# Performance work log

Hardware: AMD Instinct MI355X
Metric: run time of the kernel (lower is better)

## Reference

```python
import jax, jax.numpy as jnp
import numpy as np


def setup_inputs() -> dict:
    key = jax.random.key(0)
    B, C, H, W = 8, 64, 64, 64
    x = jax.random.normal(key, (B, C, H, W), dtype=jnp.float32)
    return {"x": x}


def reference(x) -> jnp.ndarray:
    # x: (B, C, H, W). Spatial self-attention over N = H*W positions with
    # Q = K = V = flattened x, no scaling, no projections (the Conv2d in the
    # original __init__ is never used in forward).
    B, C, H, W = x.shape
    N = H * W
    f = x.reshape(B, C, N)  # (B, C, N)
    # att[b, n, m] = sum_c f[b, c, n] * f[b, c, m]  -> (B, N, N)
    att = jnp.einsum('bcn,bcm->bnm', f, f)
    att = jax.nn.softmax(att, axis=-1)
    # outp[b, c, n] = sum_m f[b, c, m] * att[b, n, m]^T  (f_x @ att)
    outp = jnp.einsum('bcm,bmn->bcn', f, att).reshape(B, C, H, W)
    return x + outp
```

## Files before the change

### kernel.cpp

```cpp
#include <hip/hip_runtime.h>

typedef short v8s __attribute__((ext_vector_type(8)));
typedef short v4s __attribute__((ext_vector_type(4)));
typedef float v4f __attribute__((ext_vector_type(4)));

#define LOG2E 1.44269504088896340736f

#define WS_FBF_T 0u
#define WS_FBF   4194304u
#define WS_G     8388608u
#define WS_BMAX  8519680u
#define WS_NEED  8521728u

__device__ __forceinline__ unsigned short f2bf_rne(float f) {
  unsigned int u = __builtin_bit_cast(unsigned int, f);
  u += 0x7FFFu + ((u >> 16) & 1u);
  return (unsigned short)(u >> 16);
}

__global__ __launch_bounds__(256) void prep_kernel(
    const float* __restrict__ x, unsigned short* __restrict__ fbf_t,
    unsigned short* __restrict__ fbf, float* __restrict__ g, float* __restrict__ bmax) {
  __shared__ unsigned short T[64 * 72];
  __shared__ float red[16][64];
  const int t = threadIdx.x;
  const int b = blockIdx.x & 7;
  const int n0 = (blockIdx.x >> 3) << 6;
  const int nn = (t & 15) << 2;
  float ps0 = 0.f, ps1 = 0.f, ps2 = 0.f, ps3 = 0.f;
#pragma unroll
  for (int j = 0; j < 4; ++j) {
    int c = (t >> 4) + j * 16;
    size_t gidx = ((size_t)(b * 64 + c) << 12) + (unsigned)(n0 + nn);
    float4 v = *(const float4*)(x + gidx);
    ushort4 w;
    w.x = f2bf_rne(v.x); w.y = f2bf_rne(v.y); w.z = f2bf_rne(v.z); w.w = f2bf_rne(v.w);
    *(ushort4*)(fbf + gidx) = w;
    T[(nn + 0) * 72 + c] = w.x;
    T[(nn + 1) * 72 + c] = w.y;
    T[(nn + 2) * 72 + c] = w.z;
    T[(nn + 3) * 72 + c] = w.w;
    ps0 += v.x * v.x; ps1 += v.y * v.y; ps2 += v.z * v.z; ps3 += v.w * v.w;
  }
  red[t >> 4][nn + 0] = ps0; red[t >> 4][nn + 1] = ps1;
  red[t >> 4][nn + 2] = ps2; red[t >> 4][nn + 3] = ps3;
  __syncthreads();
  if (t < 64) {
    float gs = 0.f;
#pragma unroll
    for (int i = 0; i < 16; ++i) gs += red[i][t];
    g[b * 4096 + n0 + t] = gs;
    float m = gs;
    m = fmaxf(m, __shfl_xor(m, 1, 64));
    m = fmaxf(m, __shfl_xor(m, 2, 64));
    m = fmaxf(m, __shfl_xor(m, 4, 64));
    m = fmaxf(m, __shfl_xor(m, 8, 64));
    m = fmaxf(m, __shfl_xor(m, 16, 64));
    m = fmaxf(m, __shfl_xor(m, 32, 64));
    if (t == 0) bmax[b * 64 + (blockIdx.x >> 3)] = m;
  }
#pragma unroll
  for (int i = 0; i < 2; ++i) {
    int idx = t + i * 256;
    int n = idx >> 3, cs = (idx & 7) << 3;
    *(v8s*)(fbf_t + (((size_t)b << 12) + (unsigned)(n0 + n)) * 64 + cs) =
        *(const v8s*)&T[n * 72 + cs];
  }
}

__global__ __launch_bounds__(512, 2) void chanattn_main(
    const float* __restrict__ x, const unsigned short* __restrict__ fbf_t,
    const unsigned short* __restrict__ fbf, const float* __restrict__ g,
    const float* __restrict__ bmax, float* __restrict__ out) {
  __shared__ __align__(16) unsigned char smem[73728];
  unsigned short* sKtB = (unsigned short*)smem;
  unsigned short* sVcB = (unsigned short*)(smem + 18432);
  float* lred = (float*)(smem + 71680);
  const int BUF = 17920;

  const int tid = threadIdx.x;
  const int wave = tid >> 6, lane = tid & 63, quad = lane >> 4, l15 = lane & 15;
  const int qg = wave >> 2, kg = wave & 3;
  const int b = blockIdx.x & 7, qt = blockIdx.x >> 3;

  const unsigned short* fT = fbf_t + ((size_t)b << 18);
  const unsigned short* fV = fbf + ((size_t)b << 18);

  const int sKey = tid >> 3, sC = (tid & 7) << 3;
  const int vC = tid >> 4, vK = (tid & 15) << 3;
  const int vSlot = (vK & ~31) + ((vK & 8) ? 16 : 0) + ((vK & 16) ? 4 : 0);

  float gm = bmax[b * 64 + lane];
  gm = fmaxf(gm, __shfl_xor(gm, 1, 64));
  gm = fmaxf(gm, __shfl_xor(gm, 2, 64));
  gm = fmaxf(gm, __shfl_xor(gm, 4, 64));
  gm = fmaxf(gm, __shfl_xor(gm, 8, 64));
  gm = fmaxf(gm, __shfl_xor(gm, 16, 64));
  gm = fmaxf(gm, __shfl_xor(gm, 32, 64));
  float gq[4];
#pragma unroll
  for (int jq = 0; jq < 4; ++jq)
    gq[jq] = g[b * 4096 + qt * 128 + qg * 64 + jq * 16 + l15];

#pragma unroll
  for (int i = 0; i < 2; ++i)
    *(v8s*)&sKtB[(sKey + i * 64) * 72 + sC] =
        *(const v8s*)&fT[(size_t)(qt * 128 + sKey + i * 64) * 64 + sC];
  v8s pfk[2], pfv[2];
#pragma unroll
  for (int i = 0; i < 2; ++i)
    pfk[i] = *(const v8s*)&fT[(size_t)(sKey + i * 64) * 64 + sC];
#pragma unroll
  for (int i = 0; i < 2; ++i)
    pfv[i] = *(const v8s*)&fV[(size_t)(vC + i * 32) * 4096 + vK];

  __syncthreads();
  v8s bQ[4][2];
#pragma unroll
  for (int jq = 0; jq < 4; ++jq)
#pragma unroll
    for (int cs = 0; cs < 2; ++cs)
      bQ[jq][cs] = *(const v8s*)&sKtB[(qg * 64 + jq * 16 + l15) * 72 + cs * 32 + quad * 8];
  float msc[4];
#pragma unroll
  for (int jq = 0; jq < 4; ++jq) msc[jq] = __builtin_sqrtf(gq[jq] * gm) * LOG2E;
  __syncthreads();

#pragma unroll
  for (int i = 0; i < 2; ++i)
    *(v8s*)&sKtB[(sKey + i * 64) * 72 + sC] = pfk[i];
#pragma unroll
  for (int i = 0; i < 2; ++i) {
    v4s lo, hi;
#pragma unroll
    for (int j = 0; j < 4; ++j) { lo[j] = pfv[i][j]; hi[j] = pfv[i][j + 4]; }
    *(v4s*)&sVcB[(vC + i * 32) * 136 + vSlot] = lo;
    *(v4s*)&sVcB[(vC + i * 32) * 136 + vSlot + 8] = hi;
  }
#pragma unroll
  for (int i = 0; i < 2; ++i)
    pfk[i] = *(const v8s*)&fT[(size_t)(128 + sKey + i * 64) * 64 + sC];
#pragma unroll
  for (int i = 0; i < 2; ++i)
    pfv[i] = *(const v8s*)&fV[(size_t)(vC + i * 32) * 4096 + 128 + vK];

  v4f oacc[4][4];
  float rsum[4];
#pragma unroll
  for (int ct = 0; ct < 4; ++ct)
#pragma unroll
    for (int jq = 0; jq < 4; ++jq) oacc[ct][jq] = (v4f){0.f, 0.f, 0.f, 0.f};
#pragma unroll
  for (int jq = 0; jq < 4; ++jq) rsum[jq] = 0.f;

  for (int kt = 0; kt < 32; ++kt) {
    __syncthreads();
    const int po = (kt & 1) * BUF;
    const int pn = ((kt & 1) ^ 1) * BUF;

    v8s aK[2][2];
#pragma unroll
    for (int t = 0; t < 2; ++t)
#pragma unroll
      for (int cs = 0; cs < 2; ++cs)
        aK[t][cs] =
            *(const v8s*)&sKtB[po + (kg * 32 + t * 16 + l15) * 72 + cs * 32 + quad * 8];
    v8s aV[4];
#pragma unroll
    for (int ct = 0; ct < 4; ++ct)
      aV[ct] = *(const v8s*)&sVcB[po + (ct * 16 + l15) * 136 + kg * 32 + quad * 8];

    {
      const int jq = 0;
      v4f s0 = (v4f){0.f, 0.f, 0.f, 0.f}, s1 = (v4f){0.f, 0.f, 0.f, 0.f};
#pragma unroll
      for (int cs = 0; cs < 2; ++cs) {
        s0 = __builtin_amdgcn_mfma_f32_16x16x32_bf16(aK[0][cs], bQ[jq][cs], s0, 0, 0, 0);
        s1 = __builtin_amdgcn_mfma_f32_16x16x32_bf16(aK[1][cs], bQ[jq][cs], s1, 0, 0, 0);
      }
      float p0[4], p1[4];
#pragma unroll
      for (int r = 0; r < 4; ++r) {
        p0[r] = __builtin_amdgcn_exp2f(__builtin_fmaf(s0[r], LOG2E, -msc[jq]));
        p1[r] = __builtin_amdgcn_exp2f(__builtin_fmaf(s1[r], LOG2E, -msc[jq]));
      }
      rsum[jq] += ((p0[0] + p0[1]) + (p0[2] + p0[3])) +
                  ((p1[0] + p1[1]) + (p1[2] + p1[3]));
      uint4 up;
      up.x = (__builtin_bit_cast(unsigned int, p0[1]) & 0xFFFF0000u) |
             (__builtin_bit_cast(unsigned int, p0[0]) >> 16);
      up.y = (__builtin_bit_cast(unsigned int, p0[3]) & 0xFFFF0000u) |
             (__builtin_bit_cast(unsigned int, p0[2]) >> 16);
      up.z = (__builtin_bit_cast(unsigned int, p1[1]) & 0xFFFF0000u) |
             (__builtin_bit_cast(unsigned int, p1[0]) >> 16);
      up.w = (__builtin_bit_cast(unsigned int, p1[3]) & 0xFFFF0000u) |
             (__builtin_bit_cast(unsigned int, p1[2]) >> 16);
      v8s bp = __builtin_bit_cast(v8s, up);
#pragma unroll
      for (int ct = 0; ct < 4; ++ct)
        oacc[ct][jq] =
            __builtin_amdgcn_mfma_f32_16x16x32_bf16(aV[ct], bp, oacc[ct][jq], 0, 0, 0);
    }

    if (kt < 31) {
#pragma unroll
      for (int i = 0; i < 2; ++i)
        *(v8s*)&sKtB[pn + (sKey + i * 64) * 72 + sC] = pfk[i];
#pragma unroll
      for (int i = 0; i < 2; ++i) {
        v4s lo, hi;
#pragma unroll
        for (int j = 0; j < 4; ++j) { lo[j] = pfv[i][j]; hi[j] = pfv[i][j + 4]; }
        *(v4s*)&sVcB[pn + (vC + i * 32) * 136 + vSlot] = lo;
        *(v4s*)&sVcB[pn + (vC + i * 32) * 136 + vSlot + 8] = hi;
      }
    }
    if (kt < 30) {
      const int k0 = (kt + 2) << 7;
#pragma unroll
      for (int i = 0; i < 2; ++i)
        pfk[i] = *(const v8s*)&fT[(size_t)(k0 + sKey + i * 64) * 64 + sC];
#pragma unroll
      for (int i = 0; i < 2; ++i)
        pfv[i] = *(const v8s*)&fV[(size_t)(vC + i * 32) * 4096 + k0 + vK];
    }

#pragma unroll
    for (int jq = 1; jq < 4; ++jq) {
      v4f s0 = (v4f){0.f, 0.f, 0.f, 0.f}, s1 = (v4f){0.f, 0.f, 0.f, 0.f};
#pragma unroll
      for (int cs = 0; cs < 2; ++cs) {
        s0 = __builtin_amdgcn_mfma_f32_16x16x32_bf16(aK[0][cs], bQ[jq][cs], s0, 0, 0, 0);
        s1 = __builtin_amdgcn_mfma_f32_16x16x32_bf16(aK[1][cs], bQ[jq][cs], s1, 0, 0, 0);
      }
      float p0[4], p1[4];
#pragma unroll
      for (int r = 0; r < 4; ++r) {
        p0[r] = __builtin_amdgcn_exp2f(__builtin_fmaf(s0[r], LOG2E, -msc[jq]));
        p1[r] = __builtin_amdgcn_exp2f(__builtin_fmaf(s1[r], LOG2E, -msc[jq]));
      }
      rsum[jq] += ((p0[0] + p0[1]) + (p0[2] + p0[3])) +
                  ((p1[0] + p1[1]) + (p1[2] + p1[3]));
      uint4 up;
      up.x = (__builtin_bit_cast(unsigned int, p0[1]) & 0xFFFF0000u) |
             (__builtin_bit_cast(unsigned int, p0[0]) >> 16);
      up.y = (__builtin_bit_cast(unsigned int, p0[3]) & 0xFFFF0000u) |
             (__builtin_bit_cast(unsigned int, p0[2]) >> 16);
      up.z = (__builtin_bit_cast(unsigned int, p1[1]) & 0xFFFF0000u) |
             (__builtin_bit_cast(unsigned int, p1[0]) >> 16);
      up.w = (__builtin_bit_cast(unsigned int, p1[3]) & 0xFFFF0000u) |
             (__builtin_bit_cast(unsigned int, p1[2]) >> 16);
      v8s bp = __builtin_bit_cast(v8s, up);
#pragma unroll
      for (int ct = 0; ct < 4; ++ct)
        oacc[ct][jq] =
            __builtin_amdgcn_mfma_f32_16x16x32_bf16(aV[ct], bp, oacc[ct][jq], 0, 0, 0);
    }
  }

#pragma unroll
  for (int jq = 0; jq < 4; ++jq) {
    float s = rsum[jq];
    s += __shfl_xor(s, 16, 64);
    s += __shfl_xor(s, 32, 64);
    rsum[jq] = s;
  }
  if (quad == 0) {
#pragma unroll
    for (int jq = 0; jq < 4; ++jq)
      lred[(qg * 64 + jq * 16 + l15) * 4 + kg] = rsum[jq];
  }
  __syncthreads();
  float inv[4];
#pragma unroll
  for (int jq = 0; jq < 4; ++jq) {
    const float4 lv = *(const float4*)&lred[(qg * 64 + jq * 16 + l15) * 4];
    inv[jq] = __builtin_amdgcn_rcpf((lv.x + lv.y) + (lv.z + lv.w));
  }

  float* Obuf = (float*)smem;
#pragma unroll
  for (int round = 0; round < 4; ++round) {
    if (kg == round) {
#pragma unroll
      for (int ct = 0; ct < 4; ++ct)
#pragma unroll
        for (int jq = 0; jq < 4; ++jq)
#pragma unroll
          for (int r = 0; r < 4; ++r) {
            float val = oacc[ct][jq][r] * inv[jq];
            float* p = &Obuf[(qg * 64 + ct * 16 + quad * 4 + r) * 68 + jq * 16 + l15];
            if (round == 0) *p = val; else *p += val;
          }
    }
    __syncthreads();
  }
#pragma unroll
  for (int j = 0; j < 4; ++j) {
    int idx = tid + j * 512;
    int qg2 = idx >> 10, c = (idx >> 4) & 63, q4 = idx & 15;
    const float4 o = *(const float4*)&Obuf[(qg2 * 64 + c) * 68 + q4 * 4];
    size_t gidx = ((size_t)(b * 64 + c) << 12) + (unsigned)(qt * 128 + qg2 * 64 + q4 * 4);
    const float4 xv = *(const float4*)(x + gidx);
    float4 rv;
    rv.x = xv.x + o.x; rv.y = xv.y + o.y; rv.z = xv.z + o.z; rv.w = xv.w + o.w;
    *(float4*)(out + gidx) = rv;
  }
}

__global__ __launch_bounds__(512) void
chanattn_fallback(const float* __restrict__ x, float* __restrict__ out) {
  __shared__ __align__(16) unsigned char smem[54272];
  unsigned short* sKt = (unsigned short*)smem;
  unsigned short* sVc = (unsigned short*)(smem + 18432);
  unsigned short* sP  = (unsigned short*)(smem + 35840);
  const int tid = threadIdx.x;
  const int wave = tid >> 6, lane = tid & 63, quad = lane >> 4, l15 = lane & 15;
  const int b = blockIdx.x & 7, qt = blockIdx.x >> 3;
  const float* fb = x + (size_t)b * (64 * 4096);
  const int skey = tid & 127, sc0 = (tid >> 7) << 4;
  {
    float vq[16];
#pragma unroll
    for (int j = 0; j < 16; ++j) vq[j] = fb[(sc0 + j) * 4096 + qt * 128 + skey];
    unsigned short us[16];
#pragma unroll
    for (int j = 0; j < 16; ++j) us[j] = f2bf_rne(vq[j]);
#pragma unroll
    for (int h = 0; h < 2; ++h) {
      v8s t;
#pragma unroll
      for (int j = 0; j < 8; ++j) t[j] = (short)us[h * 8 + j];
      *(v8s*)&sKt[skey * 72 + sc0 + h * 8] = t;
    }
  }
  float vk[16];
#pragma unroll
  for (int j = 0; j < 16; ++j) vk[j] = fb[(sc0 + j) * 4096 + skey];
  __syncthreads();
  v8s aq[2];
#pragma unroll
  for (int cs = 0; cs < 2; ++cs)
    aq[cs] = *(const v8s*)&sKt[(wave * 16 + l15) * 72 + cs * 32 + quad * 8];
  __syncthreads();
  v4f oacc[4];
#pragma unroll
  for (int ct = 0; ct < 4; ++ct) oacc[ct] = (v4f){0.f, 0.f, 0.f, 0.f};
  float m_run[4], l_run[4];
#pragma unroll
  for (int r = 0; r < 4; ++r) { m_run[r] = -3.0e38f; l_run[r] = 0.f; }
  unsigned short* sPw = sP + wave * (16 * 72);
  for (int kt = 0; kt < 32; ++kt) {
    {
      unsigned short us[16];
#pragma unroll
      for (int j = 0; j < 16; ++j) us[j] = f2bf_rne(vk[j]);
#pragma unroll
      for (int h = 0; h < 2; ++h) {
        v8s t;
#pragma unroll
        for (int j = 0; j < 8; ++j) t[j] = (short)us[h * 8 + j];
        *(v8s*)&sKt[skey * 72 + sc0 + h * 8] = t;
      }
#pragma unroll
      for (int j = 0; j < 16; ++j) sVc[(sc0 + j) * 136 + skey] = us[j];
    }
    __syncthreads();
    if (kt + 1 < 32) {
      const int m0 = (kt + 1) * 128;
#pragma unroll
      for (int j = 0; j < 16; ++j) vk[j] = fb[(sc0 + j) * 4096 + m0 + skey];
    }
    v4f sacc[8];
#pragma unroll
    for (int t = 0; t < 8; ++t) {
      v4f acc = (v4f){0.f, 0.f, 0.f, 0.f};
#pragma unroll
      for (int cs = 0; cs < 2; ++cs) {
        v8s bf = *(const v8s*)&sKt[(t * 16 + l15) * 72 + cs * 32 + quad * 8];
        acc = __builtin_amdgcn_mfma_f32_16x16x32_bf16(aq[cs], bf, acc, 0, 0, 0);
      }
      sacc[t] = acc;
    }
    float alpha[4], msc[4], rsum[4];
#pragma unroll
    for (int r = 0; r < 4; ++r) {
      float mv = sacc[0][r];
#pragma unroll
      for (int t = 1; t < 8; ++t) mv = fmaxf(mv, sacc[t][r]);
      mv = fmaxf(mv, __shfl_xor(mv, 8, 64));
      mv = fmaxf(mv, __shfl_xor(mv, 4, 64));
      mv = fmaxf(mv, __shfl_xor(mv, 2, 64));
      mv = fmaxf(mv, __shfl_xor(mv, 1, 64));
      float mnew = fmaxf(m_run[r], mv);
      alpha[r] = __builtin_amdgcn_exp2f((m_run[r] - mnew) * LOG2E);
      m_run[r] = mnew;
      msc[r] = mnew * LOG2E;
      l_run[r] *= alpha[r];
      rsum[r] = 0.f;
    }
#pragma unroll
    for (int ct = 0; ct < 4; ++ct)
#pragma unroll
      for (int r = 0; r < 4; ++r) oacc[ct][r] *= alpha[r];
#pragma unroll
    for (int half = 0; half < 2; ++half) {
#pragma unroll
      for (int t = half * 4; t < half * 4 + 4; ++t)
#pragma unroll
        for (int r = 0; r < 4; ++r) {
          float p = __builtin_amdgcn_exp2f(__builtin_fmaf(sacc[t][r], LOG2E, -msc[r]));
          rsum[r] += p;
          sPw[(quad * 4 + r) * 72 + (t - half * 4) * 16 + l15] = f2bf_rne(p);
        }
      asm volatile("s_waitcnt lgkmcnt(0)" ::: "memory");
#pragma unroll
      for (int ms = 0; ms < 2; ++ms) {
        v8s af = *(const v8s*)&sPw[l15 * 72 + ms * 32 + quad * 8];
#pragma unroll
        for (int ct = 0; ct < 4; ++ct) {
          v8s bf = *(const v8s*)&sVc[(ct * 16 + l15) * 136 + (half * 2 + ms) * 32 + quad * 8];
          oacc[ct] = __builtin_amdgcn_mfma_f32_16x16x32_bf16(af, bf, oacc[ct], 0, 0, 0);
        }
      }
      asm volatile("s_waitcnt lgkmcnt(0)" ::: "memory");
    }
#pragma unroll
    for (int r = 0; r < 4; ++r) {
      float s = rsum[r];
      s += __shfl_xor(s, 8, 64);
      s += __shfl_xor(s, 4, 64);
      s += __shfl_xor(s, 2, 64);
      s += __shfl_xor(s, 1, 64);
      l_run[r] += s;
    }
    __syncthreads();
  }
  float inv[4];
#pragma unroll
  for (int r = 0; r < 4; ++r) inv[r] = __builtin_amdgcn_rcpf(l_run[r]);
  float* sOt = (float*)smem;
#pragma unroll
  for (int ct = 0; ct < 4; ++ct)
#pragma unroll
    for (int r = 0; r < 4; ++r)
      sOt[(ct * 16 + l15) * 132 + wave * 16 + quad * 4 + r] = oacc[ct][r] * inv[r];
  __syncthreads();
#pragma unroll
  for (int j = 0; j < 4; ++j) {
    int idx = tid + j * 512;
    int nv = idx & 31, c = idx >> 5;
    float4 o = *(const float4*)&sOt[c * 132 + nv * 4];
    size_t gaddr = (size_t)b * (64 * 4096) + (size_t)c * 4096 + (size_t)(qt * 128 + nv * 4);
    float4 xv = *(const float4*)(x + gaddr);
    float4 res = make_float4(xv.x + o.x, xv.y + o.y, xv.z + o.z, xv.w + o.w);
    *(float4*)(out + gaddr) = res;
  }
}

extern "C" void kernel_launch(void* const* d_in, const int* in_sizes, int n_in,
                              void* d_out, int out_size, void* d_ws, size_t ws_size,
                              hipStream_t stream) {
  const float* xin = (const float*)d_in[0];
  float* out = (float*)d_out;
  if (ws_size >= (size_t)WS_NEED) {
    unsigned short* fbf_t = (unsigned short*)((char*)d_ws + WS_FBF_T);
    unsigned short* fbf = (unsigned short*)((char*)d_ws + WS_FBF);
    float* g = (float*)((char*)d_ws + WS_G);
    float* bmax = (float*)((char*)d_ws + WS_BMAX);
    prep_kernel<<<dim3(512), dim3(256), 0, stream>>>(xin, fbf_t, fbf, g, bmax);
    chanattn_main<<<dim3(256), dim3(512), 0, stream>>>(xin, fbf_t, fbf, g, bmax, out);
  } else {
    chanattn_fallback<<<dim3(256), dim3(512), 0, stream>>>(xin, out);
  }
}
```

Measured before the change: 105.0 us.

## Use 1024-thread attention blocks with smaller per-wave query tiles; rewrite prep transpose

The main attention kernel now runs 1024 threads (16 waves) per block. Each wave handles 32 query rows instead of 64, which halves accumulator registers and spreads the cooperative tile loads over more threads. The prep kernel is rewritten so each thread processes one spatial position across 32 channels. That lets it write the transposed bf16 rows directly without a shared-memory transpose, and it uses 256 blocks and a 32-entry max table. Softmax probability packing now goes through a byte-permute builtin. The trade-off is one block per CU with a large shared-memory footprint, so there is less inter-block overlap, and the prep kernel's bf16 stores are strided 2-byte writes.

```diff
diff --git a/kernel.cpp b/kernel.cpp
--- a/kernel.cpp
+++ b/kernel.cpp
@@ -18,57 +18,66 @@
   return (unsigned short)(u >> 16);
 }
 
+__device__ __forceinline__ unsigned int pack_hi16(float hi, float lo) {
+#if defined(__has_builtin) && __has_builtin(__builtin_amdgcn_perm)
+  return __builtin_amdgcn_perm(__builtin_bit_cast(unsigned int, hi),
+                               __builtin_bit_cast(unsigned int, lo), 0x07060302u);
+#else
+  return (__builtin_bit_cast(unsigned int, hi) & 0xFFFF0000u) |
+         (__builtin_bit_cast(unsigned int, lo) >> 16);
+#endif
+}
+
 __global__ __launch_bounds__(256) void prep_kernel(
     const float* __restrict__ x, unsigned short* __restrict__ fbf_t,
     unsigned short* __restrict__ fbf, float* __restrict__ g, float* __restrict__ bmax) {
-  __shared__ unsigned short T[64 * 72];
-  __shared__ float red[16][64];
+  __shared__ float red[128];
+  __shared__ float wmax[2];
   const int t = threadIdx.x;
-  const int b = blockIdx.x & 7;
-  const int n0 = (blockIdx.x >> 3) << 6;
-  const int nn = (t & 15) << 2;
-  float ps0 = 0.f, ps1 = 0.f, ps2 = 0.f, ps3 = 0.f;
-#pragma unroll
-  for (int j = 0; j < 4; ++j) {
-    int c = (t >> 4) + j * 16;
-    size_t gidx = ((size_t)(b * 64 + c) << 12) + (unsigned)(n0 + nn);
-    float4 v = *(const float4*)(x + gidx);
-    ushort4 w;
-    w.x = f2bf_rne(v.x); w.y = f2bf_rne(v.y); w.z = f2bf_rne(v.z); w.w = f2bf_rne(v.w);
-    *(ushort4*)(fbf + gidx) = w;
-    T[(nn + 0) * 72 + c] = w.x;
-    T[(nn + 1) * 72 + c] = w.y;
-    T[(nn + 2) * 72 + c] = w.z;
-    T[(nn + 3) * 72 + c] = w.w;
-    ps0 += v.x * v.x; ps1 += v.y * v.y; ps2 += v.z * v.z; ps3 += v.w * v.w;
-  }
-  red[t >> 4][nn + 0] = ps0; red[t >> 4][nn + 1] = ps1;
-  red[t >> 4][nn + 2] = ps2; red[t >> 4][nn + 3] = ps3;
-  __syncthreads();
-  if (t < 64) {
-    float gs = 0.f;
-#pragma unroll
-    for (int i = 0; i < 16; ++i) gs += red[i][t];
-    g[b * 4096 + n0 + t] = gs;
-    float m = gs;
+  const int b = blockIdx.x & 7, nch = blockIdx.x >> 3;
+  const int n = (nch << 7) + (t & 127);
+  const int chalf = t >> 7, c0 = chalf << 5;
+
+  const float* xb = x + (((size_t)(b * 64 + c0)) << 12) + n;
+  unsigned short* fb = fbf + (((size_t)(b * 64 + c0)) << 12) + n;
+  float sq = 0.f;
+  unsigned int pk[16];
+#pragma unroll
+  for (int cc = 0; cc < 16; ++cc) {
+    float v0 = xb[(size_t)(2 * cc) << 12];
+    float v1 = xb[(size_t)(2 * cc + 1) << 12];
+    sq = __builtin_fmaf(v0, v0, sq);
+    sq = __builtin_fmaf(v1, v1, sq);
+    unsigned short w0 = f2bf_rne(v0), w1 = f2bf_rne(v1);
+    pk[cc] = (unsigned int)w0 | ((unsigned int)w1 << 16);
+    fb[(size_t)(2 * cc) << 12] = w0;
+    fb[(size_t)(2 * cc + 1) << 12] = w1;
+  }
+  unsigned short* ft = fbf_t + ((size_t)b << 18) + (size_t)n * 64 + c0;
+#pragma unroll
+  for (int k = 0; k < 4; ++k) {
+    uint4 u = make_uint4(pk[4 * k], pk[4 * k + 1], pk[4 * k + 2], pk[4 * k + 3]);
+    *(uint4*)(ft + k * 8) = u;
+  }
+  if (chalf == 0) red[t] = sq;
+  __syncthreads();
+  if (chalf == 1) {
+    float tot = sq + red[t & 127];
+    g[b * 4096 + n] = tot;
+    float m = tot;
     m = fmaxf(m, __shfl_xor(m, 1, 64));
     m = fmaxf(m, __shfl_xor(m, 2, 64));
     m = fmaxf(m, __shfl_xor(m, 4, 64));
     m = fmaxf(m, __shfl_xor(m, 8, 64));
     m = fmaxf(m, __shfl_xor(m, 16, 64));
     m = fmaxf(m, __shfl_xor(m, 32, 64));
-    if (t == 0) bmax[b * 64 + (blockIdx.x >> 3)] = m;
-  }
-#pragma unroll
-  for (int i = 0; i < 2; ++i) {
-    int idx = t + i * 256;
-    int n = idx >> 3, cs = (idx & 7) << 3;
-    *(v8s*)(fbf_t + (((size_t)b << 12) + (unsigned)(n0 + n)) * 64 + cs) =
-        *(const v8s*)&T[n * 72 + cs];
-  }
-}
-
-__global__ __launch_bounds__(512, 2) void chanattn_main(
+    if ((t & 63) == 0) wmax[(t >> 6) & 1] = m;
+  }
+  __syncthreads();
+  if (t == 0) bmax[b * 32 + nch] = fmaxf(wmax[0], wmax[1]);
+}
+
+__global__ __launch_bounds__(1024) void chanattn_main(
     const float* __restrict__ x, const unsigned short* __restrict__ fbf_t,
     const unsigned short* __restrict__ fbf, const float* __restrict__ g,
     const float* __restrict__ bmax, float* __restrict__ out) {
@@ -90,68 +99,52 @@
   const int vC = tid >> 4, vK = (tid & 15) << 3;
   const int vSlot = (vK & ~31) + ((vK & 8) ? 16 : 0) + ((vK & 16) ? 4 : 0);
 
-  float gm = bmax[b * 64 + lane];
+  float gm = bmax[b * 32 + (lane & 31)];
   gm = fmaxf(gm, __shfl_xor(gm, 1, 64));
   gm = fmaxf(gm, __shfl_xor(gm, 2, 64));
   gm = fmaxf(gm, __shfl_xor(gm, 4, 64));
   gm = fmaxf(gm, __shfl_xor(gm, 8, 64));
   gm = fmaxf(gm, __shfl_xor(gm, 16, 64));
-  gm = fmaxf(gm, __shfl_xor(gm, 32, 64));
-  float gq[4];
-#pragma unroll
-  for (int jq = 0; jq < 4; ++jq)
-    gq[jq] = g[b * 4096 + qt * 128 + qg * 64 + jq * 16 + l15];
-
-#pragma unroll
-  for (int i = 0; i < 2; ++i)
-    *(v8s*)&sKtB[(sKey + i * 64) * 72 + sC] =
-        *(const v8s*)&fT[(size_t)(qt * 128 + sKey + i * 64) * 64 + sC];
-  v8s pfk[2], pfv[2];
-#pragma unroll
-  for (int i = 0; i < 2; ++i)
-    pfk[i] = *(const v8s*)&fT[(size_t)(sKey + i * 64) * 64 + sC];
-#pragma unroll
-  for (int i = 0; i < 2; ++i)
-    pfv[i] = *(const v8s*)&fV[(size_t)(vC + i * 32) * 4096 + vK];
-
-  __syncthreads();
-  v8s bQ[4][2];
-#pragma unroll
-  for (int jq = 0; jq < 4; ++jq)
+  float gq[2];
+#pragma unroll
+  for (int jq = 0; jq < 2; ++jq)
+    gq[jq] = g[b * 4096 + qt * 128 + qg * 32 + jq * 16 + l15];
+
+  *(v8s*)&sKtB[sKey * 72 + sC] =
+      *(const v8s*)&fT[(size_t)(qt * 128 + sKey) * 64 + sC];
+  v8s pfk = *(const v8s*)&fT[(size_t)sKey * 64 + sC];
+  v8s pfv = *(const v8s*)&fV[(size_t)vC * 4096 + vK];
+
+  __syncthreads();
+  v8s bQ[2][2];
+#pragma unroll
+  for (int jq = 0; jq < 2; ++jq)
 #pragma unroll
     for (int cs = 0; cs < 2; ++cs)
-      bQ[jq][cs] = *(const v8s*)&sKtB[(qg * 64 + jq * 16 + l15) * 72 + cs * 32 + quad * 8];
-  float msc[4];
-#pragma unroll
-  for (int jq = 0; jq < 4; ++jq) msc[jq] = __builtin_sqrtf(gq[jq] * gm) * LOG2E;
-  __syncthreads();
-
-#pragma unroll
-  for (int i = 0; i < 2; ++i)
-    *(v8s*)&sKtB[(sKey + i * 64) * 72 + sC] = pfk[i];
-#pragma unroll
-  for (int i = 0; i < 2; ++i) {
+      bQ[jq][cs] = *(const v8s*)&sKtB[(qg * 32 + jq * 16 + l15) * 72 + cs * 32 + quad * 8];
+  float msc[2];
+#pragma unroll
+  for (int jq = 0; jq < 2; ++jq) msc[jq] = __builtin_sqrtf(gq[jq] * gm) * LOG2E;
+  __syncthreads();
+
+  *(v8s*)&sKtB[sKey * 72 + sC] = pfk;
+  {
     v4s lo, hi;
 #pragma unroll
-    for (int j = 0; j < 4; ++j) { lo[j] = pfv[i][j]; hi[j] = pfv[i][j + 4]; }
-    *(v4s*)&sVcB[(vC + i * 32) * 136 + vSlot] = lo;
-    *(v4s*)&sVcB[(vC + i * 32) * 136 + vSlot + 8] = hi;
-  }
-#pragma unroll
-  for (int i = 0; i < 2; ++i)
-    pfk[i] = *(const v8s*)&fT[(size_t)(128 + sKey + i * 64) * 64 + sC];
-#pragma unroll
-  for (int i = 0; i < 2; ++i)
-    pfv[i] = *(const v8s*)&fV[(size_t)(vC + i * 32) * 4096 + 128 + vK];
-
-  v4f oacc[4][4];
-  float rsum[4];
+    for (int j = 0; j < 4; ++j) { lo[j] = pfv[j]; hi[j] = pfv[j + 4]; }
+    *(v4s*)&sVcB[vC * 136 + vSlot] = lo;
+    *(v4s*)&sVcB[vC * 136 + vSlot + 8] = hi;
+  }
+  pfk = *(const v8s*)&fT[(size_t)(128 + sKey) * 64 + sC];
+  pfv = *(const v8s*)&fV[(size_t)vC * 4096 + 128 + vK];
+
+  v4f oacc[4][2];
+  float rsum[2];
 #pragma unroll
   for (int ct = 0; ct < 4; ++ct)
 #pragma unroll
-    for (int jq = 0; jq < 4; ++jq) oacc[ct][jq] = (v4f){0.f, 0.f, 0.f, 0.f};
-#pragma unroll
-  for (int jq = 0; jq < 4; ++jq) rsum[jq] = 0.f;
+    for (int jq = 0; jq < 2; ++jq) oacc[ct][jq] = (v4f){0.f, 0.f, 0.f, 0.f};
+  rsum[0] = 0.f; rsum[1] = 0.f;
 
   for (int kt = 0; kt < 32; ++kt) {
     __syncthreads();
@@ -187,14 +180,10 @@
       rsum[jq] += ((p0[0] + p0[1]) + (p0[2] + p0[3])) +
                   ((p1[0] + p1[1]) + (p1[2] + p1[3]));
       uint4 up;
-      up.x = (__builtin_bit_cast(unsigned int, p0[1]) & 0xFFFF0000u) |
-             (__builtin_bit_cast(unsigned int, p0[0]) >> 16);
-      up.y = (__builtin_bit_cast(unsigned int, p0[3]) & 0xFFFF0000u) |
-             (__builtin_bit_cast(unsigned int, p0[2]) >> 16);
-      up.z = (__builtin_bit_cast(unsigned int, p1[1]) & 0xFFFF0000u) |
-             (__builtin_bit_cast(unsigned int, p1[0]) >> 16);
-      up.w = (__builtin_bit_cast(unsigned int, p1[3]) & 0xFFFF0000u) |
-             (__builtin_bit_cast(unsigned int, p1[2]) >> 16);
+      up.x = pack_hi16(p0[1], p0[0]);
+      up.y = pack_hi16(p0[3], p0[2]);
+      up.z = pack_hi16(p1[1], p1[0]);
+      up.w = pack_hi16(p1[3], p1[2]);
       v8s bp = __builtin_bit_cast(v8s, up);
 #pragma unroll
       for (int ct = 0; ct < 4; ++ct)
@@ -203,30 +192,21 @@
     }
 
     if (kt < 31) {
-#pragma unroll
-      for (int i = 0; i < 2; ++i)
-        *(v8s*)&sKtB[pn + (sKey + i * 64) * 72 + sC] = pfk[i];
-#pragma unroll
-      for (int i = 0; i < 2; ++i) {
-        v4s lo, hi;
-#pragma unroll
-        for (int j = 0; j < 4; ++j) { lo[j] = pfv[i][j]; hi[j] = pfv[i][j + 4]; }
-        *(v4s*)&sVcB[pn + (vC + i * 32) * 136 + vSlot] = lo;
-        *(v4s*)&sVcB[pn + (vC + i * 32) * 136 + vSlot + 8] = hi;
-      }
+      *(v8s*)&sKtB[pn + sKey * 72 + sC] = pfk;
+      v4s lo, hi;
+#pragma unroll
+      for (int j = 0; j < 4; ++j) { lo[j] = pfv[j]; hi[j] = pfv[j + 4]; }
+      *(v4s*)&sVcB[pn + vC * 136 + vSlot] = lo;
+      *(v4s*)&sVcB[pn + vC * 136 + vSlot + 8] = hi;
     }
     if (kt < 30) {
       const int k0 = (kt + 2) << 7;
-#pragma unroll
-      for (int i = 0; i < 2; ++i)
-        pfk[i] = *(const v8s*)&fT[(size_t)(k0 + sKey + i * 64) * 64 + sC];
-#pragma unroll
-      for (int i = 0; i < 2; ++i)
-        pfv[i] = *(const v8s*)&fV[(size_t)(vC + i * 32) * 4096 + k0 + vK];
-    }
-
-#pragma unroll
-    for (int jq = 1; jq < 4; ++jq) {
+      pfk = *(const v8s*)&fT[(size_t)(k0 + sKey) * 64 + sC];
+      pfv = *(const v8s*)&fV[(size_t)vC * 4096 + k0 + vK];
+    }
+
+    {
+      const int jq = 1;
       v4f s0 = (v4f){0.f, 0.f, 0.f, 0.f}, s1 = (v4f){0.f, 0.f, 0.f, 0.f};
 #pragma unroll
       for (int cs = 0; cs < 2; ++cs) {
@@ -242,14 +222,10 @@
       rsum[jq] += ((p0[0] + p0[1]) + (p0[2] + p0[3])) +
                   ((p1[0] + p1[1]) + (p1[2] + p1[3]));
       uint4 up;
-      up.x = (__builtin_bit_cast(unsigned int, p0[1]) & 0xFFFF0000u) |
-             (__builtin_bit_cast(unsigned int, p0[0]) >> 16);
-      up.y = (__builtin_bit_cast(unsigned int, p0[3]) & 0xFFFF0000u) |
-             (__builtin_bit_cast(unsigned int, p0[2]) >> 16);
-      up.z = (__builtin_bit_cast(unsigned int, p1[1]) & 0xFFFF0000u) |
-             (__builtin_bit_cast(unsigned int, p1[0]) >> 16);
-      up.w = (__builtin_bit_cast(unsigned int, p1[3]) & 0xFFFF0000u) |
-             (__builtin_bit_cast(unsigned int, p1[2]) >> 16);
+      up.x = pack_hi16(p0[1], p0[0]);
+      up.y = pack_hi16(p0[3], p0[2]);
+      up.z = pack_hi16(p1[1], p1[0]);
+      up.w = pack_hi16(p1[3], p1[2]);
       v8s bp = __builtin_bit_cast(v8s, up);
 #pragma unroll
       for (int ct = 0; ct < 4; ++ct)
@@ -259,7 +235,7 @@
   }
 
 #pragma unroll
-  for (int jq = 0; jq < 4; ++jq) {
+  for (int jq = 0; jq < 2; ++jq) {
     float s = rsum[jq];
     s += __shfl_xor(s, 16, 64);
     s += __shfl_xor(s, 32, 64);
@@ -267,14 +243,14 @@
   }
   if (quad == 0) {
 #pragma unroll
-    for (int jq = 0; jq < 4; ++jq)
-      lred[(qg * 64 + jq * 16 + l15) * 4 + kg] = rsum[jq];
-  }
-  __syncthreads();
-  float inv[4];
-#pragma unroll
-  for (int jq = 0; jq < 4; ++jq) {
-    const float4 lv = *(const float4*)&lred[(qg * 64 + jq * 16 + l15) * 4];
+    for (int jq = 0; jq < 2; ++jq)
+      lred[(qg * 32 + jq * 16 + l15) * 4 + kg] = rsum[jq];
+  }
+  __syncthreads();
+  float inv[2];
+#pragma unroll
+  for (int jq = 0; jq < 2; ++jq) {
+    const float4 lv = *(const float4*)&lred[(qg * 32 + jq * 16 + l15) * 4];
     inv[jq] = __builtin_amdgcn_rcpf((lv.x + lv.y) + (lv.z + lv.w));
   }
 
@@ -285,22 +261,22 @@
 #pragma unroll
       for (int ct = 0; ct < 4; ++ct)
 #pragma unroll
-        for (int jq = 0; jq < 4; ++jq)
+        for (int jq = 0; jq < 2; ++jq)
 #pragma unroll
           for (int r = 0; r < 4; ++r) {
             float val = oacc[ct][jq][r] * inv[jq];
-            float* p = &Obuf[(qg * 64 + ct * 16 + quad * 4 + r) * 68 + jq * 16 + l15];
+            float* p = &Obuf[(ct * 16 + quad * 4 + r) * 132 + qg * 32 + jq * 16 + l15];
             if (round == 0) *p = val; else *p += val;
           }
     }
     __syncthreads();
   }
 #pragma unroll
-  for (int j = 0; j < 4; ++j) {
-    int idx = tid + j * 512;
-    int qg2 = idx >> 10, c = (idx >> 4) & 63, q4 = idx & 15;
-    const float4 o = *(const float4*)&Obuf[(qg2 * 64 + c) * 68 + q4 * 4];
-    size_t gidx = ((size_t)(b * 64 + c) << 12) + (unsigned)(qt * 128 + qg2 * 64 + q4 * 4);
+  for (int j = 0; j < 2; ++j) {
+    int idx = tid + j * 1024;
+    int c = idx >> 5, q4 = idx & 31;
+    const float4 o = *(const float4*)&Obuf[c * 132 + q4 * 4];
+    size_t gidx = ((size_t)(b * 64 + c) << 12) + (unsigned)(qt * 128 + q4 * 4);
     const float4 xv = *(const float4*)(x + gidx);
     float4 rv;
     rv.x = xv.x + o.x; rv.y = xv.y + o.y; rv.z = xv.z + o.z; rv.w = xv.w + o.w;
@@ -468,8 +444,8 @@
     unsigned short* fbf = (unsigned short*)((char*)d_ws + WS_FBF);
     float* g = (float*)((char*)d_ws + WS_G);
     float* bmax = (float*)((char*)d_ws + WS_BMAX);
-    prep_kernel<<<dim3(512), dim3(256), 0, stream>>>(xin, fbf_t, fbf, g, bmax);
-    chanattn_main<<<dim3(256), dim3(512), 0, stream>>>(xin, fbf_t, fbf, g, bmax, out);
+    prep_kernel<<<dim3(256), dim3(256), 0, stream>>>(xin, fbf_t, fbf, g, bmax);
+    chanattn_main<<<dim3(256), dim3(1024), 0, stream>>>(xin, fbf_t, fbf, g, bmax, out);
   } else {
     chanattn_fallback<<<dim3(256), dim3(512), 0, stream>>>(xin, out);
   }
```

New measurement: 106.5 us. Within noise of the previous version (+1.5%).

## Assign attention tiles per XCC via atomic claim and prepermute V layout in prep

Applied to the files above, without the earlier changes.

Each main-kernel block now claims a tile with an atomic CAS, starting from a range chosen by its XCC id, so that all 32 query tiles of one batch run on the same XCC and share its L2 for K/V reads. The prep kernel is rewritten to write V already in the slot-permuted layout the MFMA needs, which lets the main loop store V to LDS with a single 16-byte write instead of a split shuffle. Packing bf16 pairs now uses a v_perm builtin. The change adds a hipMemsetAsync launch and atomics, and the prep kernel now does strided 2-byte scattered global stores.

```diff
diff --git a/kernel.cpp b/kernel.cpp
--- a/kernel.cpp
+++ b/kernel.cpp
@@ -1,16 +1,16 @@
 #include <hip/hip_runtime.h>
 
 typedef short v8s __attribute__((ext_vector_type(8)));
-typedef short v4s __attribute__((ext_vector_type(4)));
 typedef float v4f __attribute__((ext_vector_type(4)));
 
 #define LOG2E 1.44269504088896340736f
 
 #define WS_FBF_T 0u
-#define WS_FBF   4194304u
+#define WS_FVP   4194304u
 #define WS_G     8388608u
 #define WS_BMAX  8519680u
-#define WS_NEED  8521728u
+#define WS_TAKEN 8521728u
+#define WS_NEED  8522752u
 
 __device__ __forceinline__ unsigned short f2bf_rne(float f) {
   unsigned int u = __builtin_bit_cast(unsigned int, f);
@@ -18,77 +18,96 @@
   return (unsigned short)(u >> 16);
 }
 
+__device__ __forceinline__ unsigned int pack_hi16(float hi, float lo) {
+#if defined(__has_builtin) && __has_builtin(__builtin_amdgcn_perm)
+  return __builtin_amdgcn_perm(__builtin_bit_cast(unsigned int, hi),
+                               __builtin_bit_cast(unsigned int, lo), 0x07060302u);
+#else
+  return (__builtin_bit_cast(unsigned int, hi) & 0xFFFF0000u) |
+         (__builtin_bit_cast(unsigned int, lo) >> 16);
+#endif
+}
+
+__device__ __forceinline__ int get_xcc_id() {
+  return (int)(__builtin_amdgcn_s_getreg((3 << 11) | 20) & 7u);
+}
+
 __global__ __launch_bounds__(256) void prep_kernel(
     const float* __restrict__ x, unsigned short* __restrict__ fbf_t,
-    unsigned short* __restrict__ fbf, float* __restrict__ g, float* __restrict__ bmax) {
-  __shared__ unsigned short T[64 * 72];
-  __shared__ float red[16][64];
+    unsigned short* __restrict__ fvp, float* __restrict__ g, float* __restrict__ bmax) {
+  __shared__ float red[4][64];
   const int t = threadIdx.x;
-  const int b = blockIdx.x & 7;
-  const int n0 = (blockIdx.x >> 3) << 6;
-  const int nn = (t & 15) << 2;
-  float ps0 = 0.f, ps1 = 0.f, ps2 = 0.f, ps3 = 0.f;
-#pragma unroll
-  for (int j = 0; j < 4; ++j) {
-    int c = (t >> 4) + j * 16;
-    size_t gidx = ((size_t)(b * 64 + c) << 12) + (unsigned)(n0 + nn);
-    float4 v = *(const float4*)(x + gidx);
-    ushort4 w;
-    w.x = f2bf_rne(v.x); w.y = f2bf_rne(v.y); w.z = f2bf_rne(v.z); w.w = f2bf_rne(v.w);
-    *(ushort4*)(fbf + gidx) = w;
-    T[(nn + 0) * 72 + c] = w.x;
-    T[(nn + 1) * 72 + c] = w.y;
-    T[(nn + 2) * 72 + c] = w.z;
-    T[(nn + 3) * 72 + c] = w.w;
-    ps0 += v.x * v.x; ps1 += v.y * v.y; ps2 += v.z * v.z; ps3 += v.w * v.w;
-  }
-  red[t >> 4][nn + 0] = ps0; red[t >> 4][nn + 1] = ps1;
-  red[t >> 4][nn + 2] = ps2; red[t >> 4][nn + 3] = ps3;
+  const int b = blockIdx.x & 7, ch = blockIdx.x >> 3;
+  const int n0 = ch << 6, nn = t & 63, n = n0 + nn, cg = t >> 6;
+
+  const int kin = nn & 31;
+  const int slot = (kin < 16) ? (((kin >> 2) << 3) + (kin & 3))
+                              : ((((kin - 16) >> 2) << 3) + ((kin - 16) & 3) + 4);
+  const int ncol = (n & ~31) + slot;
+
+  float sq = 0.f;
+  unsigned short w[16];
+#pragma unroll
+  for (int j = 0; j < 16; ++j) {
+    const int c = cg * 16 + j;
+    float v = x[((size_t)(b * 64 + c) << 12) + n];
+    sq = __builtin_fmaf(v, v, sq);
+    w[j] = f2bf_rne(v);
+  }
+  unsigned short* ft = fbf_t + ((size_t)b << 18) + (size_t)n * 64 + cg * 16;
+  *(v8s*)ft = *(v8s*)&w[0];
+  *(v8s*)(ft + 8) = *(v8s*)&w[8];
+#pragma unroll
+  for (int j = 0; j < 16; ++j)
+    fvp[((size_t)(b * 64 + cg * 16 + j) << 12) + ncol] = w[j];
+
+  red[cg][nn] = sq;
   __syncthreads();
   if (t < 64) {
-    float gs = 0.f;
-#pragma unroll
-    for (int i = 0; i < 16; ++i) gs += red[i][t];
-    g[b * 4096 + n0 + t] = gs;
-    float m = gs;
+    float tot = (red[0][t] + red[1][t]) + (red[2][t] + red[3][t]);
+    g[b * 4096 + n0 + t] = tot;
+    float m = tot;
     m = fmaxf(m, __shfl_xor(m, 1, 64));
     m = fmaxf(m, __shfl_xor(m, 2, 64));
     m = fmaxf(m, __shfl_xor(m, 4, 64));
     m = fmaxf(m, __shfl_xor(m, 8, 64));
     m = fmaxf(m, __shfl_xor(m, 16, 64));
     m = fmaxf(m, __shfl_xor(m, 32, 64));
-    if (t == 0) bmax[b * 64 + (blockIdx.x >> 3)] = m;
-  }
-#pragma unroll
-  for (int i = 0; i < 2; ++i) {
-    int idx = t + i * 256;
-    int n = idx >> 3, cs = (idx & 7) << 3;
-    *(v8s*)(fbf_t + (((size_t)b << 12) + (unsigned)(n0 + n)) * 64 + cs) =
-        *(const v8s*)&T[n * 72 + cs];
+    if (t == 0) bmax[b * 64 + ch] = m;
   }
 }
 
 __global__ __launch_bounds__(512, 2) void chanattn_main(
     const float* __restrict__ x, const unsigned short* __restrict__ fbf_t,
-    const unsigned short* __restrict__ fbf, const float* __restrict__ g,
-    const float* __restrict__ bmax, float* __restrict__ out) {
+    const unsigned short* __restrict__ fvp, const float* __restrict__ g,
+    const float* __restrict__ bmax, int* __restrict__ taken,
+    float* __restrict__ out) {
   __shared__ __align__(16) unsigned char smem[73728];
   unsigned short* sKtB = (unsigned short*)smem;
   unsigned short* sVcB = (unsigned short*)(smem + 18432);
   float* lred = (float*)(smem + 71680);
   const int BUF = 17920;
+  __shared__ int s_tile;
 
   const int tid = threadIdx.x;
   const int wave = tid >> 6, lane = tid & 63, quad = lane >> 4, l15 = lane & 15;
   const int qg = wave >> 2, kg = wave & 3;
-  const int b = blockIdx.x & 7, qt = blockIdx.x >> 3;
+
+  if (tid == 0) {
+    int start = (get_xcc_id() << 5);
+    int t = start;
+    while (atomicCAS(&taken[t], 0, 1) != 0) t = (t + 1) & 255;
+    s_tile = t;
+  }
+  __syncthreads();
+  const int tile = s_tile;
+  const int b = tile >> 5, qt = tile & 31;
 
   const unsigned short* fT = fbf_t + ((size_t)b << 18);
-  const unsigned short* fV = fbf + ((size_t)b << 18);
+  const unsigned short* fV = fvp + ((size_t)b << 18);
 
   const int sKey = tid >> 3, sC = (tid & 7) << 3;
   const int vC = tid >> 4, vK = (tid & 15) << 3;
-  const int vSlot = (vK & ~31) + ((vK & 8) ? 16 : 0) + ((vK & 16) ? 4 : 0);
 
   float gm = bmax[b * 64 + lane];
   gm = fmaxf(gm, __shfl_xor(gm, 1, 64));
@@ -130,13 +149,8 @@
   for (int i = 0; i < 2; ++i)
     *(v8s*)&sKtB[(sKey + i * 64) * 72 + sC] = pfk[i];
 #pragma unroll
-  for (int i = 0; i < 2; ++i) {
-    v4s lo, hi;
-#pragma unroll
-    for (int j = 0; j < 4; ++j) { lo[j] = pfv[i][j]; hi[j] = pfv[i][j + 4]; }
-    *(v4s*)&sVcB[(vC + i * 32) * 136 + vSlot] = lo;
-    *(v4s*)&sVcB[(vC + i * 32) * 136 + vSlot + 8] = hi;
-  }
+  for (int i = 0; i < 2; ++i)
+    *(v8s*)&sVcB[(vC + i * 32) * 136 + vK] = pfv[i];
 #pragma unroll
   for (int i = 0; i < 2; ++i)
     pfk[i] = *(const v8s*)&fT[(size_t)(128 + sKey + i * 64) * 64 + sC];
@@ -187,14 +201,10 @@
       rsum[jq] += ((p0[0] + p0[1]) + (p0[2] + p0[3])) +
                   ((p1[0] + p1[1]) + (p1[2] + p1[3]));
       uint4 up;
-      up.x = (__builtin_bit_cast(unsigned int, p0[1]) & 0xFFFF0000u) |
-             (__builtin_bit_cast(unsigned int, p0[0]) >> 16);
-      up.y = (__builtin_bit_cast(unsigned int, p0[3]) & 0xFFFF0000u) |
-             (__builtin_bit_cast(unsigned int, p0[2]) >> 16);
-      up.z = (__builtin_bit_cast(unsigned int, p1[1]) & 0xFFFF0000u) |
-             (__builtin_bit_cast(unsigned int, p1[0]) >> 16);
-      up.w = (__builtin_bit_cast(unsigned int, p1[3]) & 0xFFFF0000u) |
-             (__builtin_bit_cast(unsigned int, p1[2]) >> 16);
+      up.x = pack_hi16(p0[1], p0[0]);
+      up.y = pack_hi16(p0[3], p0[2]);
+      up.z = pack_hi16(p1[1], p1[0]);
+      up.w = pack_hi16(p1[3], p1[2]);
       v8s bp = __builtin_bit_cast(v8s, up);
 #pragma unroll
       for (int ct = 0; ct < 4; ++ct)
@@ -207,13 +217,8 @@
       for (int i = 0; i < 2; ++i)
         *(v8s*)&sKtB[pn + (sKey + i * 64) * 72 + sC] = pfk[i];
 #pragma unroll
-      for (int i = 0; i < 2; ++i) {
-        v4s lo, hi;
-#pragma unroll
-        for (int j = 0; j < 4; ++j) { lo[j] = pfv[i][j]; hi[j] = pfv[i][j + 4]; }
-        *(v4s*)&sVcB[pn + (vC + i * 32) * 136 + vSlot] = lo;
-        *(v4s*)&sVcB[pn + (vC + i * 32) * 136 + vSlot + 8] = hi;
-      }
+      for (int i = 0; i < 2; ++i)
+        *(v8s*)&sVcB[pn + (vC + i * 32) * 136 + vK] = pfv[i];
     }
     if (kt < 30) {
       const int k0 = (kt + 2) << 7;
@@ -242,14 +247,10 @@
       rsum[jq] += ((p0[0] + p0[1]) + (p0[2] + p0[3])) +
                   ((p1[0] + p1[1]) + (p1[2] + p1[3]));
       uint4 up;
-      up.x = (__builtin_bit_cast(unsigned int, p0[1]) & 0xFFFF0000u) |
-             (__builtin_bit_cast(unsigned int, p0[0]) >> 16);
-      up.y = (__builtin_bit_cast(unsigned int, p0[3]) & 0xFFFF0000u) |
-             (__builtin_bit_cast(unsigned int, p0[2]) >> 16);
-      up.z = (__builtin_bit_cast(unsigned int, p1[1]) & 0xFFFF0000u) |
-             (__builtin_bit_cast(unsigned int, p1[0]) >> 16);
-      up.w = (__builtin_bit_cast(unsigned int, p1[3]) & 0xFFFF0000u) |
-             (__builtin_bit_cast(unsigned int, p1[2]) >> 16);
+      up.x = pack_hi16(p0[1], p0[0]);
+      up.y = pack_hi16(p0[3], p0[2]);
+      up.z = pack_hi16(p1[1], p1[0]);
+      up.w = pack_hi16(p1[3], p1[2]);
       v8s bp = __builtin_bit_cast(v8s, up);
 #pragma unroll
       for (int ct = 0; ct < 4; ++ct)
@@ -465,11 +466,13 @@
   float* out = (float*)d_out;
   if (ws_size >= (size_t)WS_NEED) {
     unsigned short* fbf_t = (unsigned short*)((char*)d_ws + WS_FBF_T);
-    unsigned short* fbf = (unsigned short*)((char*)d_ws + WS_FBF);
+    unsigned short* fvp = (unsigned short*)((char*)d_ws + WS_FVP);
     float* g = (float*)((char*)d_ws + WS_G);
     float* bmax = (float*)((char*)d_ws + WS_BMAX);
-    prep_kernel<<<dim3(512), dim3(256), 0, stream>>>(xin, fbf_t, fbf, g, bmax);
-    chanattn_main<<<dim3(256), dim3(512), 0, stream>>>(xin, fbf_t, fbf, g, bmax, out);
+    int* taken = (int*)((char*)d_ws + WS_TAKEN);
+    hipMemsetAsync(taken, 0, 256 * sizeof(int), stream);
+    prep_kernel<<<dim3(512), dim3(256), 0, stream>>>(xin, fbf_t, fvp, g, bmax);
+    chanattn_main<<<dim3(256), dim3(512), 0, stream>>>(xin, fbf_t, fvp, g, bmax, taken, out);
   } else {
     chanattn_fallback<<<dim3(256), dim3(512), 0, stream>>>(xin, out);
   }
```

Result: slower. 117.0 us (+11.4%).
